# Performance work log

Hardware: AMD Instinct MI355X
Metric: run time of the kernel (lower is better)

Reference implementation:

```python
import jax, jax.numpy as jnp
import numpy as np

N_IN = 100000   # active input voxels
N_OUT = 200000  # active output voxels after stride-2 transposed conv
K = 27          # 3x3x3 kernel offsets
INC = 64
OUTC = 64
EPS = 1e-5


def setup_inputs() -> dict:
    key = jax.random.key(0)
    ks = jax.random.split(key, 6)
    return dict(
        feats=jax.random.normal(ks[0], (N_IN, INC), jnp.float32),
        weight=jax.random.normal(ks[1], (K, INC, OUTC), jnp.float32) * 0.05,
        # kernel map: per offset, which input voxel writes to which output voxel
        in_idx=jax.random.randint(ks[2], (K, N_IN), 0, N_IN, jnp.int32),
        out_idx=jax.random.randint(ks[3], (K, N_IN), 0, N_OUT, jnp.int32),
        gamma=jnp.ones((OUTC,), jnp.float32),
        beta=jnp.zeros((OUTC,), jnp.float32),
        running_mean=jax.random.normal(ks[4], (OUTC,), jnp.float32) * 0.1,
        running_var=jax.random.uniform(ks[5], (OUTC,), jnp.float32, minval=0.5, maxval=1.5),
    )


def reference(feats, weight, in_idx, out_idx, gamma, beta, running_mean, running_var):
    """Sparse transposed conv3d (gather-matmul-scatter over kernel offsets)
    followed by eval-mode BatchNorm and ReLU, matching
    torchsparse Conv3d(transposed=True) -> BatchNorm -> ReLU(inplace)."""

    def step(out, per_offset):
        w_k, ii, oi = per_offset                 # [INC,OUTC], [M], [M]
        part = feats[ii] @ w_k                   # gather + GEMM: [M, OUTC]
        return out.at[oi].add(part), None        # scatter-add into outputs

    out0 = jnp.zeros((N_OUT, OUTC), feats.dtype)
    out, _ = jax.lax.scan(step, out0, (weight, in_idx, out_idx))

    inv_std = jax.lax.rsqrt(running_var + EPS)
    y = (out - running_mean) * (inv_std * gamma) + beta
    return jax.nn.relu(y)
```

## Files before the change

### kernel.cpp

```cpp
#include <hip/hip_runtime.h>
#include <hip/hip_bf16.h>
#include <stdint.h>

#define NIN    100000
#define NOUT   200000
#define KOFF   27
#define C      64
#define NPAIR  (KOFF * NIN)
#define EPS    1e-5f
#define NCRS   391
#define CAPC   7680
#define NBIN   128
#define IPB_F  2048
#define ACW    33
#define FIXI   (1.0f / 262144.0f)

typedef __attribute__((ext_vector_type(8))) short bf16x8;
typedef __attribute__((ext_vector_type(4))) float f32x4;

__global__ __launch_bounds__(256)
void cvt_bf16_kernel(const float* __restrict__ src, ushort* __restrict__ dst, int n8)
{
    int t = blockIdx.x * 256 + threadIdx.x;
    if (t >= n8) return;
    const float4* s4 = reinterpret_cast<const float4*>(src) + (size_t)t * 2;
    float4 a = s4[0], b = s4[1];
    float v[8] = {a.x, a.y, a.z, a.w, b.x, b.y, b.z, b.w};
    union { ushort u[8]; uint4 q; } pk;
    #pragma unroll
    for (int j = 0; j < 8; ++j) {
        __hip_bfloat16 h = __float2bfloat16(v[j] * 512.0f);
        pk.u[j] = *reinterpret_cast<ushort*>(&h);
    }
    reinterpret_cast<uint4*>(dst)[t] = pk.q;
}

__global__ __launch_bounds__(256)
void cvt_wfrag_kernel(const float* __restrict__ w, ushort* __restrict__ wfrag)
{
    int t = blockIdx.x * 256 + threadIdx.x;
    if (t >= KOFF * 4 * 2 * 64) return;
    const int lane = t & 63;
    const int f    = t >> 6;
    const int kc   = f & 1;
    const int nt   = (f >> 1) & 3;
    const int k    = f >> 3;
    const int m16  = lane & 15;
    const int q    = lane >> 4;
    union { ushort u[8]; uint4 v; } pk;
    #pragma unroll
    for (int j = 0; j < 8; ++j) {
        const int ci = kc * 32 + 8 * q + j;
        const int co = nt * 16 + m16;
        __hip_bfloat16 h = __float2bfloat16(w[(size_t)k * 4096 + ci * 64 + co] * 512.0f);
        pk.u[j] = *reinterpret_cast<ushort*>(&h);
    }
    reinterpret_cast<uint4*>(wfrag)[t] = pk.v;
}

__global__ __launch_bounds__(256)
void bin_coarse_kernel(const int* __restrict__ in_idx, const int* __restrict__ out_idx,
                       int* __restrict__ gcur, uint32_t* __restrict__ binned)
{
    __shared__ uint32_t staged[IPB_F];
    __shared__ ushort   sbkt[IPB_F];
    __shared__ int hist[NCRS];
    __shared__ int lbase[NCRS];
    __shared__ int gd[NCRS];
    __shared__ int cur[NCRS];
    __shared__ int s[256];

    const int t  = threadIdx.x;
    const int t0 = blockIdx.x * IPB_F;
    int n = NPAIR - t0;
    if (n < 0) n = 0;
    if (n > IPB_F) n = IPB_F;

    for (int i = t; i < NCRS; i += 256) hist[i] = 0;
    __syncthreads();

    #pragma unroll 4
    for (int j = 0; j < IPB_F / 256; ++j) {
        int i = j * 256 + t;
        if (i < n) atomicAdd(&hist[out_idx[t0 + i] >> 9], 1);
    }
    __syncthreads();

    {
        const int i0 = 2 * t, i1 = 2 * t + 1;
        int v0 = (i0 < NCRS) ? hist[i0] : 0;
        int v1 = (i1 < NCRS) ? hist[i1] : 0;
        s[t] = v0 + v1;
        __syncthreads();
        for (int off = 1; off < 256; off <<= 1) {
            int x = (t >= off) ? s[t - off] : 0;
            __syncthreads();
            s[t] += x;
            __syncthreads();
        }
        int tb = s[t] - (v0 + v1);
        if (i0 < NCRS) lbase[i0] = tb;
        if (i1 < NCRS) lbase[i1] = tb + v0;
    }
    __syncthreads();

    for (int i = t; i < NCRS; i += 256) {
        int cnt = hist[i];
        int gb  = cnt ? atomicAdd(&gcur[i], cnt) : 0;
        gd[i]   = gb - lbase[i];
        cur[i]  = lbase[i];
    }
    __syncthreads();

    #pragma unroll 4
    for (int j = 0; j < IPB_F / 256; ++j) {
        int i = j * 256 + t;
        if (i < n) {
            int tt  = t0 + i;
            int oi  = out_idx[tt];
            int k   = tt / NIN;
            int bkt = oi >> 9;
            int pos = atomicAdd(&cur[bkt], 1);
            staged[pos] = ((uint32_t)(oi & 511) << 22)
                        | ((uint32_t)k << 17)
                        | (uint32_t)in_idx[tt];
            sbkt[pos] = (ushort)bkt;
        }
    }
    __syncthreads();

    for (int i = t; i < n; i += 256) {
        int b  = sbkt[i];
        int gp = gd[b] + i;
        if ((unsigned)gp < (unsigned)CAPC)
            binned[(size_t)b * CAPC + gp] = staged[i];
    }
}

__global__ __launch_bounds__(256)
void bin_fine_kernel(const int* __restrict__ gcur, uint32_t* __restrict__ binned,
                     int* __restrict__ foff)
{
    __shared__ uint32_t staged[CAPC];
    __shared__ int hist[NBIN], base[NBIN + 1], cur[NBIN];

    const int cb = blockIdx.x;
    const int t  = threadIdx.x;
    uint32_t* seg = binned + (size_t)cb * CAPC;
    int n = gcur[cb];
    if (n > CAPC) n = CAPC;

    if (t < NBIN) hist[t] = 0;
    __syncthreads();
    for (int i = t; i < n; i += 256) {
        uint32_t pl = seg[i];
        int b = (int)(((pl >> 29) & 3) * 32 + ((pl >> 17) & 31));
        atomicAdd(&hist[b], 1);
    }
    __syncthreads();
    if (t < NBIN) base[t + 1] = hist[t];
    __syncthreads();
    for (int off = 1; off < NBIN; off <<= 1) {
        int x = 0;
        if (t < NBIN && t >= off) x = base[t + 1 - off];
        __syncthreads();
        if (t < NBIN) base[t + 1] += x;
        __syncthreads();
    }
    if (t == 0) base[0] = 0;
    __syncthreads();
    if (t < NBIN) cur[t] = base[t + 1] - hist[t];
    __syncthreads();
    for (int i = t; i < n; i += 256) {
        uint32_t pl = seg[i];
        int b = (int)(((pl >> 29) & 3) * 32 + ((pl >> 17) & 31));
        int pos = atomicAdd(&cur[b], 1);
        staged[pos] = pl;
    }
    __syncthreads();
    for (int i = t; i < n; i += 256) seg[i] = staged[i];
    if (t <= NBIN) foff[(size_t)cb * (NBIN + 1) + t] = base[t];
}

__global__ __launch_bounds__(256)
void fused_conv_kernel(const ushort* __restrict__ featsb,
                       const ushort* __restrict__ wfragb,
                       const uint32_t* __restrict__ binned,
                       const int* __restrict__ foff,
                       const float* __restrict__ gamma,
                       const float* __restrict__ beta,
                       const float* __restrict__ mean,
                       const float* __restrict__ var,
                       float* __restrict__ out)
{
    __shared__ int acc[128 * ACW];

    const int cb   = blockIdx.x;
    const int fb   = blockIdx.y;
    const int zc   = blockIdx.z;
    const int t    = threadIdx.x;
    const int wave = t >> 6;
    const int lane = t & 63;
    const int m16  = lane & 15;
    const int q    = lane >> 4;

    for (int i = t; i < 128 * ACW; i += 256) acc[i] = 0;
    __syncthreads();

    const uint32_t* seg = binned + (size_t)cb * CAPC;
    const int* fo = foff + (size_t)cb * (NBIN + 1) + fb * 32;
    const bf16x8* wf = reinterpret_cast<const bf16x8*>(wfragb);

    for (int k = wave; k < KOFF; k += 4) {
        const int js = fo[k], je = fo[k + 1];
        if (js >= je) continue;

        bf16x8 xf[2][2];
        #pragma unroll
        for (int ntl = 0; ntl < 2; ++ntl)
            #pragma unroll
            for (int kc = 0; kc < 2; ++kc)
                xf[ntl][kc] = wf[(size_t)((k * 4 + zc * 2 + ntl) * 2 + kc) * 64 + lane];

        for (int base = js; base < je; base += 32) {
            const int idxA    = base + m16;
            const bool validA = idxA < je;
            const uint32_t plA = seg[validA ? idxA : je - 1];
            const int iiA = plA & 0x1FFFF;
            const int lrA = (int)((plA >> 22) & 127);
            const ushort* frA = featsb + (size_t)iiA * C;
            bf16x8 yA0 = *reinterpret_cast<const bf16x8*>(frA + 8 * q);
            bf16x8 yA1 = *reinterpret_cast<const bf16x8*>(frA + 32 + 8 * q);
            if (!validA) { yA0 = bf16x8{0,0,0,0,0,0,0,0}; yA1 = bf16x8{0,0,0,0,0,0,0,0}; }

            const bool doB = (base + 16) < je;
            bf16x8 yB0 = {0,0,0,0,0,0,0,0}, yB1 = {0,0,0,0,0,0,0,0};
            int lrB = 0;
            if (doB) {
                const int idxB    = base + 16 + m16;
                const bool validB = idxB < je;
                const uint32_t plB = seg[validB ? idxB : je - 1];
                const int iiB = plB & 0x1FFFF;
                lrB = (int)((plB >> 22) & 127);
                const ushort* frB = featsb + (size_t)iiB * C;
                yB0 = *reinterpret_cast<const bf16x8*>(frB + 8 * q);
                yB1 = *reinterpret_cast<const bf16x8*>(frB + 32 + 8 * q);
                if (!validB) { yB0 = bf16x8{0,0,0,0,0,0,0,0}; yB1 = bf16x8{0,0,0,0,0,0,0,0}; }
            }

            {
                f32x4 c0 = {0,0,0,0}, c1 = {0,0,0,0};
                c0 = __builtin_amdgcn_mfma_f32_16x16x32_bf16(xf[0][0], yA0, c0, 0, 0, 0);
                c1 = __builtin_amdgcn_mfma_f32_16x16x32_bf16(xf[1][0], yA0, c1, 0, 0, 0);
                c0 = __builtin_amdgcn_mfma_f32_16x16x32_bf16(xf[0][1], yA1, c0, 0, 0, 0);
                c1 = __builtin_amdgcn_mfma_f32_16x16x32_bf16(xf[1][1], yA1, c1, 0, 0, 0);
                int* arow = acc + lrA * ACW + q * 4;
                #pragma unroll
                for (int r = 0; r < 4; ++r)
                    atomicAdd(&arow[ 0 + r], __float2int_rn(c0[r]));
                #pragma unroll
                for (int r = 0; r < 4; ++r)
                    atomicAdd(&arow[16 + r], __float2int_rn(c1[r]));
            }

            if (doB) {
                f32x4 c0 = {0,0,0,0}, c1 = {0,0,0,0};
                c0 = __builtin_amdgcn_mfma_f32_16x16x32_bf16(xf[0][0], yB0, c0, 0, 0, 0);
                c1 = __builtin_amdgcn_mfma_f32_16x16x32_bf16(xf[1][0], yB0, c1, 0, 0, 0);
                c0 = __builtin_amdgcn_mfma_f32_16x16x32_bf16(xf[0][1], yB1, c0, 0, 0, 0);
                c1 = __builtin_amdgcn_mfma_f32_16x16x32_bf16(xf[1][1], yB1, c1, 0, 0, 0);
                int* arow = acc + lrB * ACW + q * 4;
                #pragma unroll
                for (int r = 0; r < 4; ++r)
                    atomicAdd(&arow[ 0 + r], __float2int_rn(c0[r]));
                #pragma unroll
                for (int r = 0; r < 4; ++r)
                    atomicAdd(&arow[16 + r], __float2int_rn(c1[r]));
            }
        }
    }
    __syncthreads();

    float4* out4 = reinterpret_cast<float4*>(out);
    #pragma unroll
    for (int rep = 0; rep < 4; ++rep) {
        const int i   = t + rep * 256;
        const int rl  = i >> 3;
        const int cp8 = i & 7;
        const int row = cb * 512 + fb * 128 + rl;
        if (row < NOUT) {
            const int c0 = zc * 32 + cp8 * 4;
            const int* ap = &acc[rl * ACW + cp8 * 4];
            float4 v;
            float* vp = reinterpret_cast<float*>(&v);
            #pragma unroll
            for (int r = 0; r < 4; ++r) {
                const int c = c0 + r;
                float s  = gamma[c] * rsqrtf(var[c] + EPS);
                float sh = beta[c] - mean[c] * s;
                float y  = fmaf((float)ap[r] * FIXI, s, sh);
                vp[r] = y > 0.f ? y : 0.f;
            }
            out4[(size_t)row * 16 + zc * 8 + cp8] = v;
        }
    }
}

__global__ __launch_bounds__(256)
void conv_scatter_kernel(const float* __restrict__ feats,
                         const float* __restrict__ weight,
                         const int*   __restrict__ in_idx,
                         const int*   __restrict__ out_idx,
                         float*       __restrict__ out)
{
    const int k    = blockIdx.y;
    const int lane = threadIdx.x & 63;
    const int wave = threadIdx.x >> 6;
    const int wavesInGrid = gridDim.x * 4;
    const int waveId      = blockIdx.x * 4 + wave;

    const float* wk = weight + (size_t)k * C * C + lane;
    float w[C];
    #pragma unroll
    for (int ci = 0; ci < C; ++ci) w[ci] = wk[(size_t)ci * C];

    const int* ii_k = in_idx  + (size_t)k * NIN;
    const int* oi_k = out_idx + (size_t)k * NIN;

    for (int r = waveId; r < NIN; r += wavesInGrid) {
        const int ii = ii_k[r];
        const int oi = oi_k[r];
        const float4* frow = reinterpret_cast<const float4*>(feats + (size_t)ii * C);
        float acc = 0.0f;
        #pragma unroll
        for (int j = 0; j < C / 4; ++j) {
            float4 f = frow[j];
            acc = fmaf(f.x, w[4 * j + 0], acc);
            acc = fmaf(f.y, w[4 * j + 1], acc);
            acc = fmaf(f.z, w[4 * j + 2], acc);
            acc = fmaf(f.w, w[4 * j + 3], acc);
        }
        atomicAdd(out + (size_t)oi * C + lane, acc);
    }
}

__global__ __launch_bounds__(256)
void bn_relu_kernel(float* __restrict__ out,
                    const float* __restrict__ gamma,
                    const float* __restrict__ beta,
                    const float* __restrict__ mean,
                    const float* __restrict__ var)
{
    const int total4 = NOUT * C / 4;
    int idx = blockIdx.x * blockDim.x + threadIdx.x;
    if (idx >= total4) return;
    const int c0 = (idx * 4) & (C - 1);
    float sc[4], sh[4];
    #pragma unroll
    for (int j = 0; j < 4; ++j) {
        const int c  = c0 + j;
        const float s = gamma[c] * rsqrtf(var[c] + EPS);
        sc[j] = s;
        sh[j] = beta[c] - mean[c] * s;
    }
    float4* p = reinterpret_cast<float4*>(out) + idx;
    float4 v = *p;
    v.x = fmaf(v.x, sc[0], sh[0]); v.x = v.x > 0.f ? v.x : 0.f;
    v.y = fmaf(v.y, sc[1], sh[1]); v.y = v.y > 0.f ? v.y : 0.f;
    v.z = fmaf(v.z, sc[2], sh[2]); v.z = v.z > 0.f ? v.z : 0.f;
    v.w = fmaf(v.w, sc[3], sh[3]); v.w = v.w > 0.f ? v.w : 0.f;
    *p = v;
}

extern "C" void kernel_launch(void* const* d_in, const int* in_sizes, int n_in,
                              void* d_out, int out_size, void* d_ws, size_t ws_size,
                              hipStream_t stream) {
    const float* feats   = (const float*)d_in[0];
    const float* weight  = (const float*)d_in[1];
    const int*   in_idx  = (const int*)  d_in[2];
    const int*   out_idx = (const int*)  d_in[3];
    const float* gamma   = (const float*)d_in[4];
    const float* beta    = (const float*)d_in[5];
    const float* rmean   = (const float*)d_in[6];
    const float* rvar    = (const float*)d_in[7];
    float* out = (float*)d_out;

    auto align = [](size_t x) { return (x + 255) & ~(size_t)255; };

    size_t a = 0;
    size_t oBin = a; a += align((size_t)NCRS * CAPC * 4);
    size_t oGc  = a; a += align((size_t)NCRS * 4);
    size_t oFo  = a; a += align((size_t)NCRS * (NBIN + 1) * 4);
    size_t oFb  = a; a += align((size_t)NIN * C * 2);
    size_t oWf  = a; a += align((size_t)KOFF * 4 * 2 * 64 * 16);

    if (ws_size < a) {
        hipMemsetAsync(out, 0, (size_t)out_size * sizeof(float), stream);
        dim3 grid(512, KOFF);
        conv_scatter_kernel<<<grid, 256, 0, stream>>>(feats, weight, in_idx, out_idx, out);
        const int total4 = NOUT * C / 4;
        bn_relu_kernel<<<(total4 + 255) / 256, 256, 0, stream>>>(out, gamma, beta, rmean, rvar);
        return;
    }

    char* ws = (char*)d_ws;
    uint32_t* binned = (uint32_t*)(ws + oBin);
    int* gcur        = (int*)(ws + oGc);
    int* foff        = (int*)(ws + oFo);
    ushort* featsb   = (ushort*)(ws + oFb);
    ushort* wfragb   = (ushort*)(ws + oWf);

    {
        int n8f = NIN * C / 8;
        cvt_bf16_kernel<<<(n8f + 255) / 256, 256, 0, stream>>>(feats, featsb, n8f);
        int nwf = KOFF * 4 * 2 * 64;
        cvt_wfrag_kernel<<<(nwf + 255) / 256, 256, 0, stream>>>(weight, wfragb);
    }

    hipMemsetAsync(gcur, 0, (size_t)NCRS * sizeof(int), stream);
    {
        int nbC = (NPAIR + IPB_F - 1) / IPB_F;
        bin_coarse_kernel<<<nbC, 256, 0, stream>>>(in_idx, out_idx, gcur, binned);
        bin_fine_kernel<<<NCRS, 256, 0, stream>>>(gcur, binned, foff);
    }

    {
        dim3 grid(NCRS, 4, 2);
        fused_conv_kernel<<<grid, 256, 0, stream>>>(featsb, wfragb, binned, foff,
                                                    gamma, beta, rmean, rvar, out);
    }
}
```

Before: 201.9 us.

## Merge output-channel halves into one block to reuse gathered features

The fused conv kernel no longer splits the 64 output channels across two z-blocks. Each block now has 512 threads (8 waves over offsets) and computes all 4 MFMA N-tiles per gathered feature row. The shared accumulator widens to 65 ints per row. This halves the redundant feature gathers, pair-list reads and block setup. In exchange it doubles per-block LDS and block size and reduces the number of blocks, which may lower occupancy. It also raises register pressure from holding 8 weight fragments.

```diff
diff --git a/kernel.cpp b/kernel.cpp
--- a/kernel.cpp
+++ b/kernel.cpp
@@ -12,7 +12,7 @@
 #define CAPC   7680
 #define NBIN   128
 #define IPB_F  2048
-#define ACW    33
+#define ACCW   65
 #define FIXI   (1.0f / 262144.0f)
 
 typedef __attribute__((ext_vector_type(8))) short bf16x8;
@@ -182,7 +182,7 @@
     if (t <= NBIN) foff[(size_t)cb * (NBIN + 1) + t] = base[t];
 }
 
-__global__ __launch_bounds__(256)
+__global__ __launch_bounds__(512)
 void fused_conv_kernel(const ushort* __restrict__ featsb,
                        const ushort* __restrict__ wfragb,
                        const uint32_t* __restrict__ binned,
@@ -193,34 +193,33 @@
                        const float* __restrict__ var,
                        float* __restrict__ out)
 {
-    __shared__ int acc[128 * ACW];
+    __shared__ int acc[128 * ACCW];
 
     const int cb   = blockIdx.x;
     const int fb   = blockIdx.y;
-    const int zc   = blockIdx.z;
     const int t    = threadIdx.x;
     const int wave = t >> 6;
     const int lane = t & 63;
     const int m16  = lane & 15;
     const int q    = lane >> 4;
 
-    for (int i = t; i < 128 * ACW; i += 256) acc[i] = 0;
+    for (int i = t; i < 128 * ACCW; i += 512) acc[i] = 0;
     __syncthreads();
 
     const uint32_t* seg = binned + (size_t)cb * CAPC;
     const int* fo = foff + (size_t)cb * (NBIN + 1) + fb * 32;
     const bf16x8* wf = reinterpret_cast<const bf16x8*>(wfragb);
 
-    for (int k = wave; k < KOFF; k += 4) {
+    for (int k = wave; k < KOFF; k += 8) {
         const int js = fo[k], je = fo[k + 1];
         if (js >= je) continue;
 
-        bf16x8 xf[2][2];
+        bf16x8 xf[4][2];
         #pragma unroll
-        for (int ntl = 0; ntl < 2; ++ntl)
+        for (int nt = 0; nt < 4; ++nt)
             #pragma unroll
             for (int kc = 0; kc < 2; ++kc)
-                xf[ntl][kc] = wf[(size_t)((k * 4 + zc * 2 + ntl) * 2 + kc) * 64 + lane];
+                xf[nt][kc] = wf[(size_t)((k * 4 + nt) * 2 + kc) * 64 + lane];
 
         for (int base = js; base < je; base += 32) {
             const int idxA    = base + m16;
@@ -249,59 +248,82 @@
             }
 
             {
-                f32x4 c0 = {0,0,0,0}, c1 = {0,0,0,0};
+                f32x4 c0 = {0,0,0,0}, c1 = {0,0,0,0}, c2 = {0,0,0,0}, c3 = {0,0,0,0};
                 c0 = __builtin_amdgcn_mfma_f32_16x16x32_bf16(xf[0][0], yA0, c0, 0, 0, 0);
                 c1 = __builtin_amdgcn_mfma_f32_16x16x32_bf16(xf[1][0], yA0, c1, 0, 0, 0);
+                c2 = __builtin_amdgcn_mfma_f32_16x16x32_bf16(xf[2][0], yA0, c2, 0, 0, 0);
+                c3 = __builtin_amdgcn_mfma_f32_16x16x32_bf16(xf[3][0], yA0, c3, 0, 0, 0);
                 c0 = __builtin_amdgcn_mfma_f32_16x16x32_bf16(xf[0][1], yA1, c0, 0, 0, 0);
                 c1 = __builtin_amdgcn_mfma_f32_16x16x32_bf16(xf[1][1], yA1, c1, 0, 0, 0);
-                int* arow = acc + lrA * ACW + q * 4;
+                c2 = __builtin_amdgcn_mfma_f32_16x16x32_bf16(xf[2][1], yA1, c2, 0, 0, 0);
+                c3 = __builtin_amdgcn_mfma_f32_16x16x32_bf16(xf[3][1], yA1, c3, 0, 0, 0);
+
+                int* arow = acc + lrA * ACCW + q * 4;
                 #pragma unroll
                 for (int r = 0; r < 4; ++r)
                     atomicAdd(&arow[ 0 + r], __float2int_rn(c0[r]));
                 #pragma unroll
                 for (int r = 0; r < 4; ++r)
                     atomicAdd(&arow[16 + r], __float2int_rn(c1[r]));
+                #pragma unroll
+                for (int r = 0; r < 4; ++r)
+                    atomicAdd(&arow[32 + r], __float2int_rn(c2[r]));
+                #pragma unroll
+                for (int r = 0; r < 4; ++r)
+                    atomicAdd(&arow[48 + r], __float2int_rn(c3[r]));
             }
 
             if (doB) {
-                f32x4 c0 = {0,0,0,0}, c1 = {0,0,0,0};
+                f32x4 c0 = {0,0,0,0}, c1 = {0,0,0,0}, c2 = {0,0,0,0}, c3 = {0,0,0,0};
                 c0 = __builtin_amdgcn_mfma_f32_16x16x32_bf16(xf[0][0], yB0, c0, 0, 0, 0);
                 c1 = __builtin_amdgcn_mfma_f32_16x16x32_bf16(xf[1][0], yB0, c1, 0, 0, 0);
+                c2 = __builtin_amdgcn_mfma_f32_16x16x32_bf16(xf[2][0], yB0, c2, 0, 0, 0);
+                c3 = __builtin_amdgcn_mfma_f32_16x16x32_bf16(xf[3][0], yB0, c3, 0, 0, 0);
                 c0 = __builtin_amdgcn_mfma_f32_16x16x32_bf16(xf[0][1], yB1, c0, 0, 0, 0);
                 c1 = __builtin_amdgcn_mfma_f32_16x16x32_bf16(xf[1][1], yB1, c1, 0, 0, 0);
-                int* arow = acc + lrB * ACW + q * 4;
+                c2 = __builtin_amdgcn_mfma_f32_16x16x32_bf16(xf[2][1], yB1, c2, 0, 0, 0);
+                c3 = __builtin_amdgcn_mfma_f32_16x16x32_bf16(xf[3][1], yB1, c3, 0, 0, 0);
+
+                int* arow = acc + lrB * ACCW + q * 4;
                 #pragma unroll
                 for (int r = 0; r < 4; ++r)
                     atomicAdd(&arow[ 0 + r], __float2int_rn(c0[r]));
                 #pragma unroll
                 for (int r = 0; r < 4; ++r)
                     atomicAdd(&arow[16 + r], __float2int_rn(c1[r]));
+                #pragma unroll
+                for (int r = 0; r < 4; ++r)
+                    atomicAdd(&arow[32 + r], __float2int_rn(c2[r]));
+                #pragma unroll
+                for (int r = 0; r < 4; ++r)
+                    atomicAdd(&arow[48 + r], __float2int_rn(c3[r]));
             }
         }
     }
     __syncthreads();
 
+    const int cp = t & 15;
+    float sc[4], sh[4];
+    #pragma unroll
+    for (int r = 0; r < 4; ++r) {
+        const int c = cp * 4 + r;
+        float s = gamma[c] * rsqrtf(var[c] + EPS);
+        sc[r] = s;
+        sh[r] = beta[c] - mean[c] * s;
+    }
     float4* out4 = reinterpret_cast<float4*>(out);
     #pragma unroll
     for (int rep = 0; rep < 4; ++rep) {
-        const int i   = t + rep * 256;
-        const int rl  = i >> 3;
-        const int cp8 = i & 7;
+        const int i   = t + rep * 512;
+        const int rl  = i >> 4;
         const int row = cb * 512 + fb * 128 + rl;
         if (row < NOUT) {
-            const int c0 = zc * 32 + cp8 * 4;
-            const int* ap = &acc[rl * ACW + cp8 * 4];
-            float4 v;
-            float* vp = reinterpret_cast<float*>(&v);
-            #pragma unroll
-            for (int r = 0; r < 4; ++r) {
-                const int c = c0 + r;
-                float s  = gamma[c] * rsqrtf(var[c] + EPS);
-                float sh = beta[c] - mean[c] * s;
-                float y  = fmaf((float)ap[r] * FIXI, s, sh);
-                vp[r] = y > 0.f ? y : 0.f;
-            }
-            out4[(size_t)row * 16 + zc * 8 + cp8] = v;
+            const int* ap = &acc[rl * ACCW + cp * 4];
+            float v0 = fmaf((float)ap[0] * FIXI, sc[0], sh[0]); v0 = v0 > 0.f ? v0 : 0.f;
+            float v1 = fmaf((float)ap[1] * FIXI, sc[1], sh[1]); v1 = v1 > 0.f ? v1 : 0.f;
+            float v2 = fmaf((float)ap[2] * FIXI, sc[2], sh[2]); v2 = v2 > 0.f ? v2 : 0.f;
+            float v3 = fmaf((float)ap[3] * FIXI, sc[3], sh[3]); v3 = v3 > 0.f ? v3 : 0.f;
+            out4[(size_t)row * 16 + cp] = make_float4(v0, v1, v2, v3);
         }
     }
 }
@@ -425,8 +447,8 @@
     }
 
     {
-        dim3 grid(NCRS, 4, 2);
-        fused_conv_kernel<<<grid, 256, 0, stream>>>(featsb, wfragb, binned, foff,
+        dim3 grid(NCRS, 4);
+        fused_conv_kernel<<<grid, 512, 0, stream>>>(featsb, wfragb, binned, foff,
                                                     gamma, beta, rmean, rvar, out);
     }
 }
```

Measured after the change: 180.7 us, median of 3. -10.5%, faster.
